# Optimization experiments

Hardware: AMD Instinct MI355X
Metric: run time of the kernel (lower is better)

Reference implementation:

```python
import jax, jax.numpy as jnp
import numpy as np

N_HEADS = 16
THETA = 10000.0

def rotate_half(x):
    x1, x2 = jnp.split(x, 2, axis=-1)
    return jnp.concatenate((-x2, x1), axis=-1)

def setup_inputs() -> dict:
    key = jax.random.key(0)
    k1, k2, k3 = jax.random.split(key, 3)
    B, T, C = 4, 2048, 2048
    x = jax.random.normal(k1, (B, T, C), dtype=jnp.float32)
    # torch Linear weights: y = x @ W.T
    wqkv = jax.random.normal(k2, (3 * C, C), dtype=jnp.float32) * (1.0 / np.sqrt(C))
    w_out = jax.random.normal(k3, (C, C), dtype=jnp.float32) * (1.0 / np.sqrt(C))
    return {"x": x, "wqkv": wqkv, "w_out": w_out}

def reference(x, wqkv, w_out):
    B, T, C = x.shape
    H = N_HEADS
    hd = C // H
    scale = 1.0 / np.sqrt(hd)

    qkv = x @ wqkv.T                               # [B, T, 3C]
    q, k, v = jnp.split(qkv, 3, axis=-1)
    q = q.reshape(B, T, H, hd).transpose(0, 2, 1, 3)  # [B, H, T, hd]
    k = k.reshape(B, T, H, hd).transpose(0, 2, 1, 3)
    v = v.reshape(B, T, H, hd).transpose(0, 2, 1, 3)

    # rotary embedding (kv_len == T, no cache)
    inv_freq = 1.0 / (THETA ** (jnp.arange(0, hd, 2, dtype=jnp.float32) / hd))
    t = jnp.arange(T, dtype=jnp.float32)
    freqs = jnp.einsum("i,j->ij", t, inv_freq)     # [T, hd/2]
    emb = jnp.concatenate((freqs, freqs), axis=-1) # [T, hd]
    cos = jnp.cos(emb)[None, None, :, :]
    sin = jnp.sin(emb)[None, None, :, :]
    q = q * cos + rotate_half(q) * sin
    k = k * cos + rotate_half(k) * sin

    scores = jnp.einsum("bhqd,bhkd->bhqk", q, k) * scale
    causal = jnp.triu(jnp.ones((T, T), dtype=bool), k=1)
    scores = jnp.where(causal[None, None], -jnp.inf, scores)
    attn = jax.nn.softmax(scores, axis=-1)
    out = jnp.einsum("bhqk,bhkd->bhqd", attn, v)   # [B, H, T, hd]
    out = out.transpose(0, 2, 1, 3).reshape(B, T, C)
    output = out @ w_out.T
    return (output, k, v)
```

## Files before the change

### kernel.cpp

```cpp
#include <hip/hip_runtime.h>

#define B_ 4
#define T_ 2048
#define C_ 2048
#define H_ 16
#define HD_ 128
#define BT_ (B_*T_)
#define N3_ (3*C_)

typedef unsigned short u16;
typedef unsigned int u32;
using short8 = __attribute__((ext_vector_type(8))) short;
using f32x4  = __attribute__((ext_vector_type(4))) float;

__device__ __forceinline__ u16 f2bf(float f) {
  union { float f; u32 u; } v; v.f = f;
  u32 r = v.u + 0x7FFFu + ((v.u >> 16) & 1u);
  return (u16)(r >> 16);
}
__device__ __forceinline__ float bf2f(u16 u) {
  union { u32 u; float f; } v; v.u = ((u32)u) << 16;
  return v.f;
}
__device__ __forceinline__ void gload_lds16(const void* g, void* l) {
  __builtin_amdgcn_global_load_lds((const __attribute__((address_space(1))) void*)g,
                                   (__attribute__((address_space(3))) void*)l, 16, 0, 0);
}

__global__ __launch_bounds__(256) void cast_f2b_kernel(const float* __restrict__ in,
                                                       u16* __restrict__ out, int n4) {
  int i = blockIdx.x * 256 + threadIdx.x;
  if (i >= n4) return;
  float4 v = ((const float4*)in)[i];
  ushort4 o;
  o.x = f2bf(v.x); o.y = f2bf(v.y); o.z = f2bf(v.z); o.w = f2bf(v.w);
  ((ushort4*)out)[i] = o;
}

__global__ __launch_bounds__(256) void rope_table_kernel(float* __restrict__ cosb,
                                                         float* __restrict__ sinb) {
  int i = blockIdx.x * 256 + threadIdx.x;
  int t = i >> 6, d = i & 63;
  float inv = powf(10000.0f, -(float)d / 64.0f);
  float ang = (float)t * inv;
  cosb[i] = cosf(ang);
  sinb[i] = sinf(ang);
}

__global__ __launch_bounds__(256) void rope_apply_kernel(const u16* __restrict__ qkv,
    const float* __restrict__ cosb, const float* __restrict__ sinb,
    u16* __restrict__ qb, u16* __restrict__ kbb,
    float* __restrict__ kout, float* __restrict__ vout) {
  int gid = blockIdx.x * 256 + threadIdx.x;
  int d = gid & 63;
  int h = (gid >> 6) & 15;
  int t = (gid >> 10) & 2047;
  int b = gid >> 21;
  const u16* row = qkv + (size_t)(b * T_ + t) * N3_;
  int base = h * HD_ + d;
  const float SCALE = 0.08838834764831845f;
  float q0 = bf2f(row[base]);
  float q1 = bf2f(row[base + 64]);
  float k0 = bf2f(row[C_ + base]);
  float k1 = bf2f(row[C_ + base + 64]);
  float v0 = bf2f(row[2*C_ + base]);
  float v1 = bf2f(row[2*C_ + base + 64]);
  float c = cosb[t * 64 + d], s = sinb[t * 64 + d];
  size_t o = ((size_t)((b * H_ + h) * T_ + t)) * HD_ + d;
  qb[o]        = f2bf((q0 * c - q1 * s) * SCALE);
  qb[o + 64]   = f2bf((q1 * c + q0 * s) * SCALE);
  float kr0 = k0 * c - k1 * s;
  float kr1 = k1 * c + k0 * s;
  kout[o]      = kr0;
  kout[o + 64] = kr1;
  kbb[o]       = f2bf(kr0);
  kbb[o + 64]  = f2bf(kr1);
  vout[o]      = v0;
  vout[o + 64] = v1;
}

__global__ __launch_bounds__(256) void vt_kernel(const u16* __restrict__ qkvb,
                                                 u16* __restrict__ vtb) {
  __shared__ u16 tile[64][72];
  int bid = blockIdx.x;
  int dh = bid & 1, tt = (bid >> 1) & 31, bh = bid >> 6;
  int b = bh >> 4, h = bh & 15;
  int tid = threadIdx.x;
  int tr = tid >> 2, tc = tid & 3;
  const u16* src = qkvb + (size_t)(b*T_ + tt*64 + tr) * N3_ + 2*C_ + h*HD_ + dh*64 + tc*16;
  short8 v0 = *(const short8*)src;
  short8 v1 = *(const short8*)(src + 8);
  #pragma unroll
  for (int j = 0; j < 8; ++j) {
    tile[tr][tc*16 + j]     = (u16)v0[j];
    tile[tr][tc*16 + 8 + j] = (u16)v1[j];
  }
  __syncthreads();
  int dr = tid >> 2, c2 = tid & 3;
  short8 o0, o1;
  #pragma unroll
  for (int j = 0; j < 8; ++j) {
    o0[j] = (short)tile[c2*16 + j][dr];
    o1[j] = (short)tile[c2*16 + 8 + j][dr];
  }
  u16* dst = vtb + ((size_t)bh * HD_ + dh*64 + dr) * T_ + tt*64 + c2*16;
  *(short8*)dst = o0;
  *(short8*)(dst + 8) = o1;
}

template<int OUT_BF16>
__global__ __launch_bounds__(512, 2) void gemm8p_kernel(const u16* __restrict__ A,
    const u16* __restrict__ Bw, void* __restrict__ Cout, int M, int N, int K, int ntx) {
  extern __shared__ u16 ldsx[];
  int lin = blockIdx.x;
  int cpx = gridDim.x >> 3;
  int wg = (lin & 7) * cpx + (lin >> 3);
  int mtile = wg / ntx, ntile = wg - mtile * ntx;
  int tid = threadIdx.x, w = tid >> 6, l = tid & 63;
  int lr = l & 15, lg = l >> 4;
  int wr = w >> 2, wc = w & 3;
  const u16* Abase = A + (size_t)mtile * 256 * K;
  const u16* Bbase = Bw + (size_t)ntile * 256 * K;

  int goff[2], ldsoff[2];
  #pragma unroll
  for (int j = 0; j < 2; ++j) {
    int s = (j*8 + w)*64 + l;
    int row = (s >> 5)*8 + (s & 7);
    int c = (s & 31) >> 3;
    goff[j] = row * K + c*8;
    ldsoff[j] = (j*8 + w) * 512;
  }
  int bbyte[4], abyte[2][4];
  #pragma unroll
  for (int n = 0; n < 4; ++n) {
    int r = wc*64 + n*16 + lr;
    bbyte[n] = ((r & ~7) << 6) + (lg << 7) + ((r & 7) << 4);
  }
  #pragma unroll
  for (int mq = 0; mq < 2; ++mq)
    #pragma unroll
    for (int m = 0; m < 4; ++m) {
      int r = wr*128 + mq*64 + m*16 + lr;
      abyte[mq][m] = ((r & ~7) << 6) + (lg << 7) + ((r & 7) << 4);
    }

  f32x4 acc[8][4];
  #pragma unroll
  for (int mi = 0; mi < 8; ++mi)
    #pragma unroll
    for (int n = 0; n < 4; ++n) acc[mi][n] = (f32x4){0.f,0.f,0.f,0.f};

  const int NT = K >> 5;
  #pragma unroll
  for (int t0 = 0; t0 < 3; ++t0) {
    const u16* ga = Abase + t0*32;
    const u16* gb = Bbase + t0*32;
    u16* la = ldsx + (size_t)t0 * 16384;
    #pragma unroll
    for (int j = 0; j < 2; ++j) gload_lds16(ga + goff[j], la + ldsoff[j]);
    #pragma unroll
    for (int j = 0; j < 2; ++j) gload_lds16(gb + goff[j], la + 8192 + ldsoff[j]);
  }
  asm volatile("s_waitcnt vmcnt(8)" ::: "memory");
  __builtin_amdgcn_s_barrier();

  for (int t = 0; t < NT; ++t) {
    const char* Al = (const char*)(ldsx + (size_t)(t & 3) * 16384);
    const char* Bl = Al + 16384;
    int tp = t + 3;
    bool stg = tp < NT;
    u16* lp = ldsx + (size_t)(tp & 3) * 16384;
    short8 bf[4], af[4];
    #pragma unroll
    for (int n = 0; n < 4; ++n) bf[n] = *(const short8*)(Bl + bbyte[n]);
    #pragma unroll
    for (int m = 0; m < 4; ++m) af[m] = *(const short8*)(Al + abyte[0][m]);
    if (stg) {
      const u16* ga = Abase + tp*32;
      #pragma unroll
      for (int j = 0; j < 2; ++j) gload_lds16(ga + goff[j], lp + ldsoff[j]);
    }
    __builtin_amdgcn_s_barrier();
    asm volatile("s_waitcnt lgkmcnt(0)" ::: "memory");
    __builtin_amdgcn_sched_barrier(0);
    __builtin_amdgcn_s_setprio(1);
    #pragma unroll
    for (int m = 0; m < 4; ++m)
      #pragma unroll
      for (int n = 0; n < 4; ++n)
        acc[m][n] = __builtin_amdgcn_mfma_f32_16x16x32_bf16(af[m], bf[n], acc[m][n], 0, 0, 0);
    __builtin_amdgcn_s_setprio(0);
    __builtin_amdgcn_s_barrier();
    #pragma unroll
    for (int m = 0; m < 4; ++m) af[m] = *(const short8*)(Al + abyte[1][m]);
    if (stg) {
      const u16* gb = Bbase + tp*32;
      #pragma unroll
      for (int j = 0; j < 2; ++j) gload_lds16(gb + goff[j], lp + 8192 + ldsoff[j]);
    }
    if (t + 3 < NT)      { asm volatile("s_waitcnt vmcnt(8)" ::: "memory"); }
    else if (t + 2 < NT) { asm volatile("s_waitcnt vmcnt(4)" ::: "memory"); }
    else                 { asm volatile("s_waitcnt vmcnt(0)" ::: "memory"); }
    __builtin_amdgcn_s_barrier();
    asm volatile("s_waitcnt lgkmcnt(0)" ::: "memory");
    __builtin_amdgcn_sched_barrier(0);
    __builtin_amdgcn_s_setprio(1);
    #pragma unroll
    for (int m = 0; m < 4; ++m)
      #pragma unroll
      for (int n = 0; n < 4; ++n)
        acc[4+m][n] = __builtin_amdgcn_mfma_f32_16x16x32_bf16(af[m], bf[n], acc[4+m][n], 0, 0, 0);
    __builtin_amdgcn_s_setprio(0);
    __builtin_amdgcn_s_barrier();
  }
  #pragma unroll
  for (int mi = 0; mi < 8; ++mi)
    #pragma unroll
    for (int n = 0; n < 4; ++n)
      #pragma unroll
      for (int r = 0; r < 4; ++r) {
        int grow = mtile*256 + wr*128 + mi*16 + lg*4 + r;
        int gcol = ntile*256 + wc*64 + n*16 + lr;
        float v = acc[mi][n][r];
        if (OUT_BF16) ((u16*)Cout)[(size_t)grow * N + gcol] = f2bf(v);
        else          ((float*)Cout)[(size_t)grow * N + gcol] = v;
      }
}

struct TileSt {
  short8 aq[4];
  f32x4 oacc[8];
  float m_run[4];
  float l_run[4];
};

__device__ __forceinline__ void stage_kv(const u16* kpl, const u16* vpl, int kt,
                                         u16* Kd, u16* Vd, int w, int l) {
  const u16* kTile = kpl + (size_t)kt * 64 * HD_;
  int ktOff = kt * 64;
  #pragma unroll
  for (int j = 0; j < 4; ++j) {
    int s = (j*4 + w)*64 + l;
    int g = s ^ ((s >> 4) & 7);
    gload_lds16(kTile + (g >> 4)*HD_ + (g & 15)*8, (char*)Kd + (j*4 + w)*1024);
    int g2 = s ^ ((s >> 3) & 7);
    gload_lds16(vpl + (size_t)(g2 >> 3)*T_ + ktOff + (g2 & 7)*8, (char*)Vd + (j*4 + w)*1024);
  }
}

__device__ __forceinline__ void attn_tile(TileSt& st, const u16* Kl, const u16* Vl,
                                          char* Pw, bool diag, int lr, int lg, int w) {
  f32x4 s_acc[4];
  #pragma unroll
  for (int ct = 0; ct < 4; ++ct) s_acc[ct] = (f32x4){0.f, 0.f, 0.f, 0.f};
  __builtin_amdgcn_s_setprio(1);
  #pragma unroll
  for (int kg = 0; kg < 4; ++kg) {
    #pragma unroll
    for (int ct = 0; ct < 4; ++ct) {
      int krow = ct*16 + lr;
      int kbyte = (krow*256 + (kg*32 + lg*8)*2) ^ ((krow & 7) << 4);
      short8 bk = *(const short8*)((const char*)Kl + kbyte);
      s_acc[ct] = __builtin_amdgcn_mfma_f32_16x16x32_bf16(st.aq[kg], bk, s_acc[ct], 0, 0, 0);
    }
  }
  __builtin_amdgcn_s_setprio(0);
  float p[4][4];
  #pragma unroll
  for (int ct = 0; ct < 4; ++ct)
    #pragma unroll
    for (int r = 0; r < 4; ++r) {
      float sv = s_acc[ct][r];
      if (diag && (ct*16 + lr) > (w*16 + lg*4 + r)) sv = -INFINITY;
      p[ct][r] = sv;
    }
  float fac[4];
  #pragma unroll
  for (int r = 0; r < 4; ++r) {
    float mx = fmaxf(fmaxf(p[0][r], p[1][r]), fmaxf(p[2][r], p[3][r]));
    #pragma unroll
    for (int off = 1; off < 16; off <<= 1) mx = fmaxf(mx, __shfl_xor(mx, off));
    float mn = fmaxf(st.m_run[r], mx);
    fac[r] = __expf(st.m_run[r] - mn);
    st.m_run[r] = mn;
    float ls = 0.f;
    #pragma unroll
    for (int ct = 0; ct < 4; ++ct) { float pv = __expf(p[ct][r] - mn); p[ct][r] = pv; ls += pv; }
    #pragma unroll
    for (int off = 1; off < 16; off <<= 1) ls += __shfl_xor(ls, off);
    st.l_run[r] = st.l_run[r] * fac[r] + ls;
  }
  #pragma unroll
  for (int dt = 0; dt < 8; ++dt)
    #pragma unroll
    for (int r = 0; r < 4; ++r) st.oacc[dt][r] *= fac[r];
  #pragma unroll
  for (int ct = 0; ct < 4; ++ct)
    #pragma unroll
    for (int r = 0; r < 4; ++r) {
      int prow = lg*4 + r;
      int pb = (prow*128 + (ct*16 + lr)*2) ^ ((prow & 7) << 4);
      *(u16*)(Pw + pb) = f2bf(p[ct][r]);
    }
  asm volatile("s_waitcnt lgkmcnt(0)" ::: "memory");
  __builtin_amdgcn_sched_barrier(0);
  short8 pa[2];
  #pragma unroll
  for (int kk = 0; kk < 2; ++kk) {
    int pb = (lr*128 + (kk*32 + lg*8)*2) ^ ((lr & 7) << 4);
    pa[kk] = *(const short8*)(Pw + pb);
  }
  __builtin_amdgcn_s_setprio(1);
  #pragma unroll
  for (int dt = 0; dt < 8; ++dt) {
    #pragma unroll
    for (int kk = 0; kk < 2; ++kk) {
      int vrow = dt*16 + lr;
      int vbyte = (vrow*128 + (kk*32 + lg*8)*2) ^ ((vrow & 7) << 4);
      short8 bv = *(const short8*)((const char*)Vl + vbyte);
      st.oacc[dt] = __builtin_amdgcn_mfma_f32_16x16x32_bf16(pa[kk], bv, st.oacc[dt], 0, 0, 0);
    }
  }
  __builtin_amdgcn_s_setprio(0);
}

__device__ __forceinline__ void write_out(TileSt& st, u16* __restrict__ ao,
                                          int b, int h, int qbase, int lr, int lg, int w) {
  float invl[4];
  #pragma unroll
  for (int r = 0; r < 4; ++r) invl[r] = 1.0f / st.l_run[r];
  #pragma unroll
  for (int dt = 0; dt < 8; ++dt)
    #pragma unroll
    for (int r = 0; r < 4; ++r) {
      int t = qbase + w*16 + lg*4 + r;
      int col = h*HD_ + dt*16 + lr;
      ao[(size_t)(b * T_ + t) * C_ + col] = f2bf(st.oacc[dt][r] * invl[r]);
    }
}

__global__ __launch_bounds__(256, 2) void attn_kernel(const u16* __restrict__ qb,
    const u16* __restrict__ kb, const u16* __restrict__ vtb, u16* __restrict__ ao) {
  __shared__ u16 Kl[2][64 * 128];
  __shared__ u16 Vl[2][128 * 64];
  __shared__ u16 Pl[4][16 * 64];
  int bid0 = blockIdx.x;
  int bid = (bid0 & 7) * 128 + (bid0 >> 3);
  int bh = bid >> 4, pr = bid & 15;
  int lo = pr, hi = 31 - pr;
  int b = bh >> 4, h = bh & 15;
  int tid = threadIdx.x, w = tid >> 6, l = tid & 63;
  int lr = l & 15, lg = l >> 4;
  const u16* qptr = qb + (size_t)bh * T_ * HD_;
  const u16* kpl  = kb + (size_t)bh * T_ * HD_;
  const u16* vpl  = vtb + (size_t)bh * HD_ * T_;
  char* Pw = (char*)&Pl[w][0];

  TileSt stL, stH;
  #pragma unroll
  for (int kg = 0; kg < 4; ++kg) {
    stL.aq[kg] = *(const short8*)(qptr + (size_t)(lo*64 + w*16 + lr) * HD_ + kg*32 + lg*8);
    stH.aq[kg] = *(const short8*)(qptr + (size_t)(hi*64 + w*16 + lr) * HD_ + kg*32 + lg*8);
  }
  #pragma unroll
  for (int dt = 0; dt < 8; ++dt) {
    stL.oacc[dt] = (f32x4){0.f, 0.f, 0.f, 0.f};
    stH.oacc[dt] = (f32x4){0.f, 0.f, 0.f, 0.f};
  }
  #pragma unroll
  for (int r = 0; r < 4; ++r) {
    stL.m_run[r] = -INFINITY; stH.m_run[r] = -INFINITY;
    stL.l_run[r] = 0.f;       stH.l_run[r] = 0.f;
  }

  stage_kv(kpl, vpl, 0, &Kl[0][0], &Vl[0][0], w, l);
  __syncthreads();
  int cur = 0;
  for (int kt = 0; kt <= hi; ++kt) {
    if (kt < hi) stage_kv(kpl, vpl, kt + 1, &Kl[cur ^ 1][0], &Vl[cur ^ 1][0], w, l);
    attn_tile(stH, &Kl[cur][0], &Vl[cur][0], Pw, kt == hi, lr, lg, w);
    if (kt <= lo) attn_tile(stL, &Kl[cur][0], &Vl[cur][0], Pw, kt == lo, lr, lg, w);
    __syncthreads();
    cur ^= 1;
  }
  write_out(stH, ao, b, h, hi*64, lr, lg, w);
  write_out(stL, ao, b, h, lo*64, lr, lg, w);
}

extern "C" void kernel_launch(void* const* d_in, const int* in_sizes, int n_in,
                              void* d_out, int out_size, void* d_ws, size_t ws_size,
                              hipStream_t stream) {
  const float* x     = (const float*)d_in[0];
  const float* wqkv  = (const float*)d_in[1];
  const float* w_out = (const float*)d_in[2];
  float* out = (float*)d_out;

  char* ws = (char*)d_ws;
  size_t off = 0;
  u16* xb    = (u16*)(ws + off); off += (size_t)BT_ * C_ * 2;
  u16* wqkvb = (u16*)(ws + off); off += (size_t)N3_ * C_ * 2;
  u16* woutb = (u16*)(ws + off); off += (size_t)C_ * C_ * 2;
  u16* qkvb  = (u16*)(ws + off); off += (size_t)BT_ * N3_ * 2;
  u16* qbf   = (u16*)(ws + off); off += (size_t)BT_ * C_ * 2;
  u16* aob   = (u16*)(ws + off); off += (size_t)BT_ * C_ * 2;
  u16* kbb   = (u16*)(ws + off); off += (size_t)BT_ * C_ * 2;
  u16* vtb   = (u16*)(ws + off); off += (size_t)BT_ * C_ * 2;
  float* cosb = (float*)(ws + off); off += (size_t)T_ * 64 * 4;
  float* sinb = (float*)(ws + off); off += (size_t)T_ * 64 * 4;

  float* kout = out + (size_t)BT_ * C_;
  float* vout = out + 2 * (size_t)BT_ * C_;

  hipFuncSetAttribute((const void*)gemm8p_kernel<1>,
                      hipFuncAttributeMaxDynamicSharedMemorySize, 131072);
  hipFuncSetAttribute((const void*)gemm8p_kernel<0>,
                      hipFuncAttributeMaxDynamicSharedMemorySize, 131072);

  cast_f2b_kernel<<<(BT_*C_/4)/256, 256, 0, stream>>>(x, xb, BT_*C_/4);
  cast_f2b_kernel<<<(N3_*C_/4)/256, 256, 0, stream>>>(wqkv, wqkvb, N3_*C_/4);
  cast_f2b_kernel<<<(C_*C_/4)/256, 256, 0, stream>>>(w_out, woutb, C_*C_/4);
  rope_table_kernel<<<(T_*64)/256, 256, 0, stream>>>(cosb, sinb);
  gemm8p_kernel<1><<<(N3_/256)*(BT_/256), 512, 131072, stream>>>(xb, wqkvb, qkvb, BT_, N3_, C_, N3_/256);
  rope_apply_kernel<<<(B_*T_*H_*64)/256, 256, 0, stream>>>(qkvb, cosb, sinb, qbf, kbb, kout, vout);
  vt_kernel<<<B_*H_*(T_/64)*2, 256, 0, stream>>>(qkvb, vtb);
  attn_kernel<<<B_*H_*16, 256, 0, stream>>>(qbf, kbb, vtb, aob);
  gemm8p_kernel<0><<<(C_/256)*(BT_/256), 512, 131072, stream>>>(aob, woutb, out, BT_, C_, C_, C_/256);
}
```

Measured before the change: 571.7 us.

## Rewrite bf16 GEMM main loop as 2-stage K=64 pipeline with quadrant MFMA schedule

The GEMM kernel now stages 64-wide K tiles into two LDS buffers instead of 32-wide tiles into four ring buffers. The LDS layout for A and B halves is also reorganised. The main loop splits each wave's 128x64 output into quadrants. LDS fragment reads for the next quadrant and global-to-LDS staging of tile T+2 are interleaved between MFMA bursts, aiming to hide load latency and cut barriers per unit of K. In exchange, the prefetch distance is shallower and there are more live fragment registers.

```diff
diff --git a/kernel.cpp b/kernel.cpp
--- a/kernel.cpp
+++ b/kernel.cpp
@@ -109,7 +109,7 @@
 }
 
 template<int OUT_BF16>
-__global__ __launch_bounds__(512, 2) void gemm8p_kernel(const u16* __restrict__ A,
+__global__ __launch_bounds__(512, 2) void gemm3p_kernel(const u16* __restrict__ A,
     const u16* __restrict__ Bw, void* __restrict__ Cout, int M, int N, int K, int ntx) {
   extern __shared__ u16 ldsx[];
   int lin = blockIdx.x;
@@ -122,28 +122,63 @@
   const u16* Abase = A + (size_t)mtile * 256 * K;
   const u16* Bbase = Bw + (size_t)ntile * 256 * K;
 
-  int goff[2], ldsoff[2];
+  int srow[2], scol[2], sdst[2];
   #pragma unroll
   for (int j = 0; j < 2; ++j) {
-    int s = (j*8 + w)*64 + l;
-    int row = (s >> 5)*8 + (s & 7);
-    int c = (s & 31) >> 3;
-    goff[j] = row * K + c*8;
-    ldsoff[j] = (j*8 + w) * 512;
-  }
-  int bbyte[4], abyte[2][4];
-  #pragma unroll
-  for (int n = 0; n < 4; ++n) {
-    int r = wc*64 + n*16 + lr;
-    bbyte[n] = ((r & ~7) << 6) + (lg << 7) + ((r & 7) << 4);
-  }
-  #pragma unroll
-  for (int mq = 0; mq < 2; ++mq)
-    #pragma unroll
-    for (int m = 0; m < 4; ++m) {
-      int r = wr*128 + mq*64 + m*16 + lr;
-      abyte[mq][m] = ((r & ~7) << 6) + (lg << 7) + ((r & 7) << 4);
-    }
+    int s = j*512 + tid;
+    srow[j] = (s >> 6)*8 + (s & 7);
+    scol[j] = ((s >> 3) & 7) * 8;
+    sdst[j] = s * 8;
+  }
+  int arow[8], brow[4];
+  #pragma unroll
+  for (int mi = 0; mi < 8; ++mi) {
+    int rho = mi*16 + lr;
+    arow[mi] = (rho >> 3)*512 + (rho & 7)*8 + lg*64;
+  }
+  #pragma unroll
+  for (int nj = 0; nj < 4; ++nj) {
+    int rho = (wc & 1)*64 + nj*16 + lr;
+    brow[nj] = (rho >> 3)*512 + (rho & 7)*8 + lg*64;
+  }
+  const int haOff = (2 + wr) * 8192;
+  const int hbOff = (wc >> 1) * 8192;
+
+  auto stageB = [&](int Tp) {
+    u16* dst = ldsx + (Tp & 1) * 32768;
+    const u16* g = Bbase + Tp * 64;
+    #pragma unroll
+    for (int j = 0; j < 2; ++j)
+      gload_lds16(g + (size_t)srow[j] * K + scol[j], dst + sdst[j]);
+    #pragma unroll
+    for (int j = 0; j < 2; ++j)
+      gload_lds16(g + (size_t)(128 + srow[j]) * K + scol[j], dst + 8192 + sdst[j]);
+  };
+  auto stageA = [&](int Tp) {
+    u16* dst = ldsx + (Tp & 1) * 32768 + 16384;
+    const u16* g = Abase + Tp * 64;
+    #pragma unroll
+    for (int j = 0; j < 2; ++j)
+      gload_lds16(g + (size_t)srow[j] * K + scol[j], dst + sdst[j]);
+    #pragma unroll
+    for (int j = 0; j < 2; ++j)
+      gload_lds16(g + (size_t)(128 + srow[j]) * K + scol[j], dst + 8192 + sdst[j]);
+  };
+
+  short8 am03[4][2], am47[4][2], bn01[2][2], bn23[2][2];
+  auto readQ0 = [&](int T) {
+    const u16* base = ldsx + (T & 1) * 32768;
+    #pragma unroll
+    for (int i = 0; i < 4; ++i)
+      #pragma unroll
+      for (int kk = 0; kk < 2; ++kk)
+        am03[i][kk] = *(const short8*)(base + haOff + arow[i] + kk*256);
+    #pragma unroll
+    for (int j = 0; j < 2; ++j)
+      #pragma unroll
+      for (int kk = 0; kk < 2; ++kk)
+        bn01[j][kk] = *(const short8*)(base + hbOff + brow[j] + kk*256);
+  };
 
   f32x4 acc[8][4];
   #pragma unroll
@@ -151,67 +186,74 @@
     #pragma unroll
     for (int n = 0; n < 4; ++n) acc[mi][n] = (f32x4){0.f,0.f,0.f,0.f};
 
-  const int NT = K >> 5;
-  #pragma unroll
-  for (int t0 = 0; t0 < 3; ++t0) {
-    const u16* ga = Abase + t0*32;
-    const u16* gb = Bbase + t0*32;
-    u16* la = ldsx + (size_t)t0 * 16384;
-    #pragma unroll
-    for (int j = 0; j < 2; ++j) gload_lds16(ga + goff[j], la + ldsoff[j]);
-    #pragma unroll
-    for (int j = 0; j < 2; ++j) gload_lds16(gb + goff[j], la + 8192 + ldsoff[j]);
-  }
+  const int NT = K >> 6;
+  stageB(0); stageA(0); stageB(1); stageA(1);
   asm volatile("s_waitcnt vmcnt(8)" ::: "memory");
+  __builtin_amdgcn_sched_barrier(0);
   __builtin_amdgcn_s_barrier();
-
-  for (int t = 0; t < NT; ++t) {
-    const char* Al = (const char*)(ldsx + (size_t)(t & 3) * 16384);
-    const char* Bl = Al + 16384;
-    int tp = t + 3;
-    bool stg = tp < NT;
-    u16* lp = ldsx + (size_t)(tp & 3) * 16384;
-    short8 bf[4], af[4];
-    #pragma unroll
-    for (int n = 0; n < 4; ++n) bf[n] = *(const short8*)(Bl + bbyte[n]);
-    #pragma unroll
-    for (int m = 0; m < 4; ++m) af[m] = *(const short8*)(Al + abyte[0][m]);
+  readQ0(0);
+
+  for (int T = 0; T < NT; ++T) {
+    const u16* base = ldsx + (T & 1) * 32768;
+    bool stg = (T + 2) < NT;
+    #pragma unroll
+    for (int j = 0; j < 2; ++j)
+      #pragma unroll
+      for (int kk = 0; kk < 2; ++kk)
+        bn23[j][kk] = *(const short8*)(base + hbOff + brow[2+j] + kk*256);
+    __builtin_amdgcn_s_barrier();
+    __builtin_amdgcn_s_setprio(1);
+    #pragma unroll
+    for (int i = 0; i < 4; ++i)
+      #pragma unroll
+      for (int jj = 0; jj < 2; ++jj)
+        #pragma unroll
+        for (int kk = 0; kk < 2; ++kk)
+          acc[i][jj] = __builtin_amdgcn_mfma_f32_16x16x32_bf16(am03[i][kk], bn01[jj][kk], acc[i][jj], 0, 0, 0);
+    __builtin_amdgcn_s_setprio(0);
+    __builtin_amdgcn_s_barrier();
+    if (stg) stageB(T + 2);
+    #pragma unroll
+    for (int i = 0; i < 4; ++i)
+      #pragma unroll
+      for (int kk = 0; kk < 2; ++kk)
+        am47[i][kk] = *(const short8*)(base + haOff + arow[4+i] + kk*256);
+    __builtin_amdgcn_s_barrier();
+    __builtin_amdgcn_s_setprio(1);
+    #pragma unroll
+    for (int i = 0; i < 4; ++i)
+      #pragma unroll
+      for (int jj = 0; jj < 2; ++jj)
+        #pragma unroll
+        for (int kk = 0; kk < 2; ++kk)
+          acc[i][2+jj] = __builtin_amdgcn_mfma_f32_16x16x32_bf16(am03[i][kk], bn23[jj][kk], acc[i][2+jj], 0, 0, 0);
+    __builtin_amdgcn_s_setprio(0);
+    __builtin_amdgcn_s_barrier();
     if (stg) {
-      const u16* ga = Abase + tp*32;
-      #pragma unroll
-      for (int j = 0; j < 2; ++j) gload_lds16(ga + goff[j], lp + ldsoff[j]);
-    }
-    __builtin_amdgcn_s_barrier();
-    asm volatile("s_waitcnt lgkmcnt(0)" ::: "memory");
+      stageA(T + 2);
+      asm volatile("s_waitcnt vmcnt(8)" ::: "memory");
+    } else {
+      asm volatile("s_waitcnt vmcnt(0)" ::: "memory");
+    }
     __builtin_amdgcn_sched_barrier(0);
+    __builtin_amdgcn_s_barrier();
     __builtin_amdgcn_s_setprio(1);
     #pragma unroll
-    for (int m = 0; m < 4; ++m)
-      #pragma unroll
-      for (int n = 0; n < 4; ++n)
-        acc[m][n] = __builtin_amdgcn_mfma_f32_16x16x32_bf16(af[m], bf[n], acc[m][n], 0, 0, 0);
+    for (int i = 0; i < 4; ++i)
+      #pragma unroll
+      for (int jj = 0; jj < 2; ++jj)
+        #pragma unroll
+        for (int kk = 0; kk < 2; ++kk)
+          acc[4+i][2+jj] = __builtin_amdgcn_mfma_f32_16x16x32_bf16(am47[i][kk], bn23[jj][kk], acc[4+i][2+jj], 0, 0, 0);
+    #pragma unroll
+    for (int i = 0; i < 4; ++i)
+      #pragma unroll
+      for (int jj = 0; jj < 2; ++jj)
+        #pragma unroll
+        for (int kk = 0; kk < 2; ++kk)
+          acc[4+i][jj] = __builtin_amdgcn_mfma_f32_16x16x32_bf16(am47[i][kk], bn01[jj][kk], acc[4+i][jj], 0, 0, 0);
     __builtin_amdgcn_s_setprio(0);
-    __builtin_amdgcn_s_barrier();
-    #pragma unroll
-    for (int m = 0; m < 4; ++m) af[m] = *(const short8*)(Al + abyte[1][m]);
-    if (stg) {
-      const u16* gb = Bbase + tp*32;
-      #pragma unroll
-      for (int j = 0; j < 2; ++j) gload_lds16(gb + goff[j], lp + 8192 + ldsoff[j]);
-    }
-    if (t + 3 < NT)      { asm volatile("s_waitcnt vmcnt(8)" ::: "memory"); }
-    else if (t + 2 < NT) { asm volatile("s_waitcnt vmcnt(4)" ::: "memory"); }
-    else                 { asm volatile("s_waitcnt vmcnt(0)" ::: "memory"); }
-    __builtin_amdgcn_s_barrier();
-    asm volatile("s_waitcnt lgkmcnt(0)" ::: "memory");
-    __builtin_amdgcn_sched_barrier(0);
-    __builtin_amdgcn_s_setprio(1);
-    #pragma unroll
-    for (int m = 0; m < 4; ++m)
-      #pragma unroll
-      for (int n = 0; n < 4; ++n)
-        acc[4+m][n] = __builtin_amdgcn_mfma_f32_16x16x32_bf16(af[m], bf[n], acc[4+m][n], 0, 0, 0);
-    __builtin_amdgcn_s_setprio(0);
+    if (T + 1 < NT) readQ0(T + 1);
     __builtin_amdgcn_s_barrier();
   }
   #pragma unroll
@@ -412,18 +454,18 @@
   float* kout = out + (size_t)BT_ * C_;
   float* vout = out + 2 * (size_t)BT_ * C_;
 
-  hipFuncSetAttribute((const void*)gemm8p_kernel<1>,
+  hipFuncSetAttribute((const void*)gemm3p_kernel<1>,
                       hipFuncAttributeMaxDynamicSharedMemorySize, 131072);
-  hipFuncSetAttribute((const void*)gemm8p_kernel<0>,
+  hipFuncSetAttribute((const void*)gemm3p_kernel<0>,
                       hipFuncAttributeMaxDynamicSharedMemorySize, 131072);
 
   cast_f2b_kernel<<<(BT_*C_/4)/256, 256, 0, stream>>>(x, xb, BT_*C_/4);
   cast_f2b_kernel<<<(N3_*C_/4)/256, 256, 0, stream>>>(wqkv, wqkvb, N3_*C_/4);
   cast_f2b_kernel<<<(C_*C_/4)/256, 256, 0, stream>>>(w_out, woutb, C_*C_/4);
   rope_table_kernel<<<(T_*64)/256, 256, 0, stream>>>(cosb, sinb);
-  gemm8p_kernel<1><<<(N3_/256)*(BT_/256), 512, 131072, stream>>>(xb, wqkvb, qkvb, BT_, N3_, C_, N3_/256);
+  gemm3p_kernel<1><<<(N3_/256)*(BT_/256), 512, 131072, stream>>>(xb, wqkvb, qkvb, BT_, N3_, C_, N3_/256);
   rope_apply_kernel<<<(B_*T_*H_*64)/256, 256, 0, stream>>>(qkvb, cosb, sinb, qbf, kbb, kout, vout);
   vt_kernel<<<B_*H_*(T_/64)*2, 256, 0, stream>>>(qkvb, vtb);
   attn_kernel<<<B_*H_*16, 256, 0, stream>>>(qbf, kbb, vtb, aob);
-  gemm8p_kernel<0><<<(C_/256)*(BT_/256), 512, 131072, stream>>>(aob, woutb, out, BT_, C_, C_, C_/256);
-}
+  gemm3p_kernel<0><<<(C_/256)*(BT_/256), 512, 131072, stream>>>(aob, woutb, out, BT_, C_, C_, C_/256);
+}
```

Measured after the change: 575.3 us. No clear change (+0.6%).
